# Kernel optimization log

Hardware: AMD Instinct MI355X
Metric: run time of the kernel (lower is better)

## Reference

```python
import jax, jax.numpy as jnp
import numpy as np

N_NODES = 50000
N_EDGES = 640000
IN_CH = 128
OUT_CH = 128


def setup_inputs() -> dict:
    key = jax.random.key(0)
    k1, k2, k3, k4 = jax.random.split(key, 4)
    x = jax.random.normal(k1, (N_NODES, IN_CH), dtype=jnp.float32)
    edge_index = jax.random.randint(k2, (2, N_EDGES), 0, N_NODES, dtype=jnp.int32)
    # nn.Linear params: W [out, in], b [out]
    bound = 1.0 / np.sqrt(IN_CH)
    W = jax.random.uniform(k3, (OUT_CH, IN_CH), minval=-bound, maxval=bound, dtype=jnp.float32)
    b = jax.random.uniform(k4, (OUT_CH,), minval=-bound, maxval=bound, dtype=jnp.float32)
    return {"x": x, "edge_index": edge_index, "W": W, "b": b}


def reference(x, edge_index, W, b):
    row, col = edge_index[0], edge_index[1]
    num_nodes = x.shape[0]
    # degree of each destination node (clamped to >= 1)
    deg = jax.ops.segment_sum(jnp.ones(row.shape[0], dtype=x.dtype), row,
                              num_segments=num_nodes)
    deg = jnp.maximum(deg, 1.0)
    # gather neighbor features and scatter-add into destinations
    agg = jax.ops.segment_sum(x[col], row, num_segments=num_nodes)
    agg = agg / deg[:, None]
    # residual + linear
    return (x + agg) @ W.T + b
```

## Files before the change

kernel.cpp:

```cpp
#include <hip/hip_runtime.h>

#define N_NODES 50000
#define N_EDGES 640000
#define CH 128
#define NBINS 391
#define CAPB 32
#define CAP2 5024
#define CAPR 48
#define NTILES 1563
#define FILLB 157

typedef __bf16 bf16_t;
typedef bf16_t bf16x8 __attribute__((ext_vector_type(8)));
typedef float f32x4 __attribute__((ext_vector_type(4)));

__device__ __forceinline__ ushort f2bf(float f) {
  union { float f; unsigned u; } v; v.f = f;
  unsigned r = v.u + 0x7FFFu + ((v.u >> 16) & 1u);
  return (ushort)(r >> 16);
}
__device__ __forceinline__ float bflo(unsigned u) {
  union { unsigned u; float f; } v; v.u = u << 16; return v.f;
}
__device__ __forceinline__ float bfhi(unsigned u) {
  union { unsigned u; float f; } v; v.u = u & 0xFFFF0000u; return v.f;
}
__device__ __forceinline__ unsigned pack2(float lo, float hi) {
  return (unsigned)f2bf(lo) | ((unsigned)f2bf(hi) << 16);
}


__global__ __launch_bounds__(256) void fill_conv(const int* __restrict__ row,
                                                 const int* __restrict__ col,
                                                 unsigned* __restrict__ binArr,
                                                 const float4* __restrict__ x4,
                                                 uint4* __restrict__ xb4,
                                                 const float4* __restrict__ W4,
                                                 uint4* __restrict__ Wb4) {
  int bid = blockIdx.x;
  int tid = threadIdx.x;
  if (bid < FILLB) {
    __shared__ int lh[NBINS];
    for (int i = tid; i < NBINS; i += 256) lh[i] = 0;
    __syncthreads();
    int base = bid * 4096 + tid * 16;
    bool act = base < N_EDGES;
    int rr[16], cc[16], bi[16], rk[16];
    if (act) {
#pragma unroll
      for (int u = 0; u < 4; ++u) {
        int4 r4 = *(const int4*)(row + base + u * 4);
        int4 c4 = *(const int4*)(col + base + u * 4);
        rr[u * 4 + 0] = r4.x; rr[u * 4 + 1] = r4.y; rr[u * 4 + 2] = r4.z; rr[u * 4 + 3] = r4.w;
        cc[u * 4 + 0] = c4.x; cc[u * 4 + 1] = c4.y; cc[u * 4 + 2] = c4.z; cc[u * 4 + 3] = c4.w;
      }
#pragma unroll
      for (int i = 0; i < 16; ++i) {
        bi[i] = rr[i] >> 7;
        rk[i] = atomicAdd(&lh[bi[i]], 1);
      }
#pragma unroll
      for (int i = 0; i < 16; ++i) {
        if (rk[i] < CAPB) {
          binArr[bi[i] * CAP2 + bid * CAPB + rk[i]] =
              ((unsigned)(rr[i] & 127) << 16) | (unsigned)cc[i];
        }
      }
    }
  } else if (bid < FILLB + 3125) {
    int i = (bid - FILLB) * 256 + tid;
    float4 a = x4[i * 2], b = x4[i * 2 + 1];
    uint4 o;
    o.x = pack2(a.x, a.y); o.y = pack2(a.z, a.w);
    o.z = pack2(b.x, b.y); o.w = pack2(b.z, b.w);
    xb4[i] = o;
  } else {
    for (int i = tid; i < 2048; i += 256) {
      float4 c = W4[i * 2], d = W4[i * 2 + 1];
      uint4 w;
      w.x = pack2(c.x, c.y); w.y = pack2(c.z, c.w);
      w.z = pack2(d.x, d.y); w.w = pack2(d.z, d.w);
      Wb4[i] = w;
    }
  }
}

__global__ __launch_bounds__(256) void fused(const uint4* __restrict__ xb4,
                                             const uint4* __restrict__ binArr4,
                                             const uint4* __restrict__ Wb4,
                                             const float4* __restrict__ bias4,
                                             float4* __restrict__ out4) {
  __shared__ ushort hT[32 * CH];
  __shared__ ushort colL[32 * CAPR];
  __shared__ int rowcnt[32];
  int tid = threadIdx.x;
  int g = blockIdx.x;
  int m0 = g * 32;

  if (tid < 32) rowcnt[tid] = 0;
  __syncthreads();
  {
    int b = g >> 2;
    unsigned sub = (unsigned)(g & 3);
    const uint4* seg4 = binArr4 + b * (CAP2 / 4);
    for (int j = tid; j < CAP2 / 4; j += 256) {
      uint4 rv = seg4[j];
      unsigned recs[4] = {rv.x, rv.y, rv.z, rv.w};
#pragma unroll
      for (int i = 0; i < 4; ++i) {
        unsigned rec = recs[i];
        if ((rec >> 21) == sub) {
          int lr = (rec >> 16) & 31;
          int p = atomicAdd(&rowcnt[lr], 1);
          if (p < CAPR) colL[lr * CAPR + p] = (ushort)(rec & 0xFFFFu);
        }
      }
    }
  }
  __syncthreads();

  int wv = tid >> 6;
  int lane = tid & 63;
  int q = lane & 15;
  int grp = lane >> 4;
#pragma unroll
  for (int t = 0; t < 2; ++t) {
    int r = wv * 8 + t * 4 + grp;
    int node = m0 + r;
    int deg = rowcnt[r];
    int degc = deg < CAPR ? deg : CAPR;
    const ushort* arow = colL + r * CAPR;
    float acc[8] = {0.f, 0.f, 0.f, 0.f, 0.f, 0.f, 0.f, 0.f};
    int e = 0;
    for (; e + 3 < degc; e += 4) {
      uint2 ids = *(const uint2*)(arow + e);
      int n0 = ids.x & 0xFFFF, n1 = ids.x >> 16;
      int n2 = ids.y & 0xFFFF, n3 = ids.y >> 16;
      uint4 v0 = xb4[n0 * 16 + q];
      uint4 v1 = xb4[n1 * 16 + q];
      uint4 v2 = xb4[n2 * 16 + q];
      uint4 v3 = xb4[n3 * 16 + q];
      acc[0] += bflo(v0.x); acc[1] += bfhi(v0.x); acc[2] += bflo(v0.y); acc[3] += bfhi(v0.y);
      acc[4] += bflo(v0.z); acc[5] += bfhi(v0.z); acc[6] += bflo(v0.w); acc[7] += bfhi(v0.w);
      acc[0] += bflo(v1.x); acc[1] += bfhi(v1.x); acc[2] += bflo(v1.y); acc[3] += bfhi(v1.y);
      acc[4] += bflo(v1.z); acc[5] += bfhi(v1.z); acc[6] += bflo(v1.w); acc[7] += bfhi(v1.w);
      acc[0] += bflo(v2.x); acc[1] += bfhi(v2.x); acc[2] += bflo(v2.y); acc[3] += bfhi(v2.y);
      acc[4] += bflo(v2.z); acc[5] += bfhi(v2.z); acc[6] += bflo(v2.w); acc[7] += bfhi(v2.w);
      acc[0] += bflo(v3.x); acc[1] += bfhi(v3.x); acc[2] += bflo(v3.y); acc[3] += bfhi(v3.y);
      acc[4] += bflo(v3.z); acc[5] += bfhi(v3.z); acc[6] += bflo(v3.w); acc[7] += bfhi(v3.w);
    }
    for (; e < degc; ++e) {
      int nb = arow[e];
      uint4 v = xb4[nb * 16 + q];
      acc[0] += bflo(v.x); acc[1] += bfhi(v.x); acc[2] += bflo(v.y); acc[3] += bfhi(v.y);
      acc[4] += bflo(v.z); acc[5] += bfhi(v.z); acc[6] += bflo(v.w); acc[7] += bfhi(v.w);
    }
    uint4 o = make_uint4(0, 0, 0, 0);
    if (node < N_NODES) {
      float s = 1.0f / fmaxf((float)deg, 1.0f);
      uint4 xi = xb4[node * 16 + q];
      o.x = pack2(bflo(xi.x) + acc[0] * s, bfhi(xi.x) + acc[1] * s);
      o.y = pack2(bflo(xi.y) + acc[2] * s, bfhi(xi.y) + acc[3] * s);
      o.z = pack2(bflo(xi.z) + acc[4] * s, bfhi(xi.z) + acc[5] * s);
      o.w = pack2(bflo(xi.w) + acc[6] * s, bfhi(xi.w) + acc[7] * s);
    }
    *(uint4*)&hT[r * CH + q * 8] = o;
  }
  __syncthreads();

  int qq = grp;
  int mt = wv & 1;
  int nbase = (wv >> 1) * 4;
  const ushort* hrow = &hT[(mt * 16 + q) * CH + qq * 8];
  bf16x8 hb0 = *(const bf16x8*)(hrow);
  bf16x8 hb1 = *(const bf16x8*)(hrow + 32);
  bf16x8 hb2 = *(const bf16x8*)(hrow + 64);
  bf16x8 hb3 = *(const bf16x8*)(hrow + 96);
  int m = m0 + mt * 16 + q;
#pragma unroll
  for (int i = 0; i < 4; ++i) {
    int nt = nbase + i;
    const uint4* wr = Wb4 + (nt * 16 + q) * 16 + qq;
    bf16x8 w0 = __builtin_bit_cast(bf16x8, wr[0]);
    bf16x8 w1 = __builtin_bit_cast(bf16x8, wr[4]);
    bf16x8 w2 = __builtin_bit_cast(bf16x8, wr[8]);
    bf16x8 w3 = __builtin_bit_cast(bf16x8, wr[12]);
    f32x4 acc = {0.f, 0.f, 0.f, 0.f};
    acc = __builtin_amdgcn_mfma_f32_16x16x32_bf16(w0, hb0, acc, 0, 0, 0);
    acc = __builtin_amdgcn_mfma_f32_16x16x32_bf16(w1, hb1, acc, 0, 0, 0);
    acc = __builtin_amdgcn_mfma_f32_16x16x32_bf16(w2, hb2, acc, 0, 0, 0);
    acc = __builtin_amdgcn_mfma_f32_16x16x32_bf16(w3, hb3, acc, 0, 0, 0);
    if (m < N_NODES) {
      float4 bv = bias4[nt * 4 + qq];
      float4 o;
      o.x = acc[0] + bv.x;
      o.y = acc[1] + bv.y;
      o.z = acc[2] + bv.z;
      o.w = acc[3] + bv.w;
      out4[(size_t)m * 32 + nt * 4 + qq] = o;
    }
  }
}

extern "C" void kernel_launch(void* const* d_in, const int* in_sizes, int n_in,
                              void* d_out, int out_size, void* d_ws, size_t ws_size,
                              hipStream_t stream) {
  const float* x  = (const float*)d_in[0];
  const int*   ei = (const int*)d_in[1];
  const float* W  = (const float*)d_in[2];
  const float* bb = (const float*)d_in[3];

  char* ws = (char*)d_ws;
  unsigned* binArr = (unsigned*)ws;
  uint4*    Wb4    = (uint4*)(ws + 7857536);
  uint4*    xb4    = (uint4*)(ws + 7890304);

  fill_conv<<<FILLB + 3125 + 1, 256, 0, stream>>>(ei, ei + N_EDGES, binArr,
                                                  (const float4*)x, xb4,
                                                  (const float4*)W, Wb4);
  fused<<<NTILES, 256, 0, stream>>>(xb4, (const uint4*)binArr, Wb4,
                                    (const float4*)bb, (float4*)d_out);
}
```

Baseline: 127.1 us.

## Interleave two-row neighbor gathers, swizzle LDS tile, add nontemporal loads/stores

Each thread now gathers neighbors for its two destination rows in one interleaved loop, so up to eight independent row loads are in flight instead of four. The self-feature load is hoisted ahead of the loop. The hT shared tile uses an XOR swizzle on the 16-byte chunk index to reduce LDS bank conflicts on the MFMA operand reads. Bin records are read and output is written with nontemporal hints to limit cache pollution. The costs are predication overhead when the two rows have unequal degrees, and higher register pressure.

Measured after the change: 132.9 us. +4.6%, slower.

```diff
diff --git a/kernel.cpp b/kernel.cpp
--- a/kernel.cpp
+++ b/kernel.cpp
@@ -13,6 +13,7 @@
 typedef __bf16 bf16_t;
 typedef bf16_t bf16x8 __attribute__((ext_vector_type(8)));
 typedef float f32x4 __attribute__((ext_vector_type(4)));
+typedef unsigned u32x4 __attribute__((ext_vector_type(4)));
 
 __device__ __forceinline__ ushort f2bf(float f) {
   union { float f; unsigned u; } v; v.f = f;
@@ -27,6 +28,12 @@
 }
 __device__ __forceinline__ unsigned pack2(float lo, float hi) {
   return (unsigned)f2bf(lo) | ((unsigned)f2bf(hi) << 16);
+}
+__device__ __forceinline__ void addrow(float* acc, uint4 v) {
+  acc[0] += bflo(v.x); acc[1] += bfhi(v.x);
+  acc[2] += bflo(v.y); acc[3] += bfhi(v.y);
+  acc[4] += bflo(v.z); acc[5] += bfhi(v.z);
+  acc[6] += bflo(v.w); acc[7] += bfhi(v.w);
 }
 
 
@@ -102,9 +109,9 @@
   {
     int b = g >> 2;
     unsigned sub = (unsigned)(g & 3);
-    const uint4* seg4 = binArr4 + b * (CAP2 / 4);
+    const u32x4* seg4 = (const u32x4*)(binArr4 + b * (CAP2 / 4));
     for (int j = tid; j < CAP2 / 4; j += 256) {
-      uint4 rv = seg4[j];
+      u32x4 rv = __builtin_nontemporal_load(seg4 + j);
       unsigned recs[4] = {rv.x, rv.y, rv.z, rv.w};
 #pragma unroll
       for (int i = 0; i < 4; ++i) {
@@ -123,59 +130,89 @@
   int lane = tid & 63;
   int q = lane & 15;
   int grp = lane >> 4;
-#pragma unroll
-  for (int t = 0; t < 2; ++t) {
-    int r = wv * 8 + t * 4 + grp;
-    int node = m0 + r;
-    int deg = rowcnt[r];
-    int degc = deg < CAPR ? deg : CAPR;
-    const ushort* arow = colL + r * CAPR;
-    float acc[8] = {0.f, 0.f, 0.f, 0.f, 0.f, 0.f, 0.f, 0.f};
-    int e = 0;
-    for (; e + 3 < degc; e += 4) {
-      uint2 ids = *(const uint2*)(arow + e);
-      int n0 = ids.x & 0xFFFF, n1 = ids.x >> 16;
-      int n2 = ids.y & 0xFFFF, n3 = ids.y >> 16;
-      uint4 v0 = xb4[n0 * 16 + q];
-      uint4 v1 = xb4[n1 * 16 + q];
-      uint4 v2 = xb4[n2 * 16 + q];
-      uint4 v3 = xb4[n3 * 16 + q];
-      acc[0] += bflo(v0.x); acc[1] += bfhi(v0.x); acc[2] += bflo(v0.y); acc[3] += bfhi(v0.y);
-      acc[4] += bflo(v0.z); acc[5] += bfhi(v0.z); acc[6] += bflo(v0.w); acc[7] += bfhi(v0.w);
-      acc[0] += bflo(v1.x); acc[1] += bfhi(v1.x); acc[2] += bflo(v1.y); acc[3] += bfhi(v1.y);
-      acc[4] += bflo(v1.z); acc[5] += bfhi(v1.z); acc[6] += bflo(v1.w); acc[7] += bfhi(v1.w);
-      acc[0] += bflo(v2.x); acc[1] += bfhi(v2.x); acc[2] += bflo(v2.y); acc[3] += bfhi(v2.y);
-      acc[4] += bflo(v2.z); acc[5] += bfhi(v2.z); acc[6] += bflo(v2.w); acc[7] += bfhi(v2.w);
-      acc[0] += bflo(v3.x); acc[1] += bfhi(v3.x); acc[2] += bflo(v3.y); acc[3] += bfhi(v3.y);
-      acc[4] += bflo(v3.z); acc[5] += bfhi(v3.z); acc[6] += bflo(v3.w); acc[7] += bfhi(v3.w);
-    }
-    for (; e < degc; ++e) {
-      int nb = arow[e];
-      uint4 v = xb4[nb * 16 + q];
-      acc[0] += bflo(v.x); acc[1] += bfhi(v.x); acc[2] += bflo(v.y); acc[3] += bfhi(v.y);
-      acc[4] += bflo(v.z); acc[5] += bfhi(v.z); acc[6] += bflo(v.w); acc[7] += bfhi(v.w);
-    }
-    uint4 o = make_uint4(0, 0, 0, 0);
-    if (node < N_NODES) {
-      float s = 1.0f / fmaxf((float)deg, 1.0f);
-      uint4 xi = xb4[node * 16 + q];
-      o.x = pack2(bflo(xi.x) + acc[0] * s, bfhi(xi.x) + acc[1] * s);
-      o.y = pack2(bflo(xi.y) + acc[2] * s, bfhi(xi.y) + acc[3] * s);
-      o.z = pack2(bflo(xi.z) + acc[4] * s, bfhi(xi.z) + acc[5] * s);
-      o.w = pack2(bflo(xi.w) + acc[6] * s, bfhi(xi.w) + acc[7] * s);
-    }
-    *(uint4*)&hT[r * CH + q * 8] = o;
+  int r0 = wv * 8 + grp;
+  int r1 = r0 + 4;
+  int node0 = m0 + r0, node1 = m0 + r1;
+  int deg0 = rowcnt[r0], deg1 = rowcnt[r1];
+  int dc0 = deg0 < CAPR ? deg0 : CAPR;
+  int dc1 = deg1 < CAPR ? deg1 : CAPR;
+  const ushort* a0 = colL + r0 * CAPR;
+  const ushort* a1 = colL + r1 * CAPR;
+  int n0c = node0 < N_NODES ? node0 : 0;
+  int n1c = node1 < N_NODES ? node1 : 0;
+  uint4 xi0 = xb4[n0c * 16 + q];
+  uint4 xi1 = xb4[n1c * 16 + q];
+  float acc0[8] = {0.f, 0.f, 0.f, 0.f, 0.f, 0.f, 0.f, 0.f};
+  float acc1[8] = {0.f, 0.f, 0.f, 0.f, 0.f, 0.f, 0.f, 0.f};
+  int e0 = 0, e1 = 0;
+  while ((e0 + 3 < dc0) | (e1 + 3 < dc1)) {
+    bool p0 = e0 + 3 < dc0;
+    bool p1 = e1 + 3 < dc1;
+    uint4 v00, v01, v02, v03, v10, v11, v12, v13;
+    if (p0) {
+      uint2 id0 = *(const uint2*)(a0 + e0);
+      v00 = xb4[(id0.x & 0xFFFF) * 16 + q];
+      v01 = xb4[(id0.x >> 16) * 16 + q];
+      v02 = xb4[(id0.y & 0xFFFF) * 16 + q];
+      v03 = xb4[(id0.y >> 16) * 16 + q];
+    }
+    if (p1) {
+      uint2 id1 = *(const uint2*)(a1 + e1);
+      v10 = xb4[(id1.x & 0xFFFF) * 16 + q];
+      v11 = xb4[(id1.x >> 16) * 16 + q];
+      v12 = xb4[(id1.y & 0xFFFF) * 16 + q];
+      v13 = xb4[(id1.y >> 16) * 16 + q];
+    }
+    if (p0) {
+      addrow(acc0, v00); addrow(acc0, v01);
+      addrow(acc0, v02); addrow(acc0, v03);
+      e0 += 4;
+    }
+    if (p1) {
+      addrow(acc1, v10); addrow(acc1, v11);
+      addrow(acc1, v12); addrow(acc1, v13);
+      e1 += 4;
+    }
+  }
+  while ((e0 < dc0) | (e1 < dc1)) {
+    bool p0 = e0 < dc0;
+    bool p1 = e1 < dc1;
+    uint4 v0, v1;
+    if (p0) v0 = xb4[(int)a0[e0] * 16 + q];
+    if (p1) v1 = xb4[(int)a1[e1] * 16 + q];
+    if (p0) { addrow(acc0, v0); ++e0; }
+    if (p1) { addrow(acc1, v1); ++e1; }
+  }
+  {
+    uint4 o0 = make_uint4(0, 0, 0, 0);
+    if (node0 < N_NODES) {
+      float s = 1.0f / fmaxf((float)deg0, 1.0f);
+      o0.x = pack2(bflo(xi0.x) + acc0[0] * s, bfhi(xi0.x) + acc0[1] * s);
+      o0.y = pack2(bflo(xi0.y) + acc0[2] * s, bfhi(xi0.y) + acc0[3] * s);
+      o0.z = pack2(bflo(xi0.z) + acc0[4] * s, bfhi(xi0.z) + acc0[5] * s);
+      o0.w = pack2(bflo(xi0.w) + acc0[6] * s, bfhi(xi0.w) + acc0[7] * s);
+    }
+    *(uint4*)&hT[r0 * CH + ((q ^ (r0 & 15)) << 3)] = o0;
+    uint4 o1 = make_uint4(0, 0, 0, 0);
+    if (node1 < N_NODES) {
+      float s = 1.0f / fmaxf((float)deg1, 1.0f);
+      o1.x = pack2(bflo(xi1.x) + acc1[0] * s, bfhi(xi1.x) + acc1[1] * s);
+      o1.y = pack2(bflo(xi1.y) + acc1[2] * s, bfhi(xi1.y) + acc1[3] * s);
+      o1.z = pack2(bflo(xi1.z) + acc1[4] * s, bfhi(xi1.z) + acc1[5] * s);
+      o1.w = pack2(bflo(xi1.w) + acc1[6] * s, bfhi(xi1.w) + acc1[7] * s);
+    }
+    *(uint4*)&hT[r1 * CH + ((q ^ (r1 & 15)) << 3)] = o1;
   }
   __syncthreads();
 
   int qq = grp;
   int mt = wv & 1;
   int nbase = (wv >> 1) * 4;
-  const ushort* hrow = &hT[(mt * 16 + q) * CH + qq * 8];
-  bf16x8 hb0 = *(const bf16x8*)(hrow);
-  bf16x8 hb1 = *(const bf16x8*)(hrow + 32);
-  bf16x8 hb2 = *(const bf16x8*)(hrow + 64);
-  bf16x8 hb3 = *(const bf16x8*)(hrow + 96);
+  const ushort* hbase = &hT[(mt * 16 + q) * CH];
+  bf16x8 hb0 = *(const bf16x8*)(hbase + (((qq + 0) ^ q) << 3));
+  bf16x8 hb1 = *(const bf16x8*)(hbase + (((qq + 4) ^ q) << 3));
+  bf16x8 hb2 = *(const bf16x8*)(hbase + (((qq + 8) ^ q) << 3));
+  bf16x8 hb3 = *(const bf16x8*)(hbase + (((qq + 12) ^ q) << 3));
   int m = m0 + mt * 16 + q;
 #pragma unroll
   for (int i = 0; i < 4; ++i) {
@@ -192,12 +229,12 @@
     acc = __builtin_amdgcn_mfma_f32_16x16x32_bf16(w3, hb3, acc, 0, 0, 0);
     if (m < N_NODES) {
       float4 bv = bias4[nt * 4 + qq];
-      float4 o;
+      f32x4 o;
       o.x = acc[0] + bv.x;
       o.y = acc[1] + bv.y;
       o.z = acc[2] + bv.z;
       o.w = acc[3] + bv.w;
-      out4[(size_t)m * 32 + nt * 4 + qq] = o;
+      __builtin_nontemporal_store(o, (f32x4*)(out4 + (size_t)m * 32 + nt * 4 + qq));
     }
   }
 }
```
